# Performance work log

Hardware: AMD Instinct MI355X
Metric: run time of the kernel (lower is better)

## Reference

```python
import jax, jax.numpy as jnp
import numpy as np

N = 32768
F0, F1, F2, F3 = 16, 32, 64, 128
D0, D1, D2, D3 = (128, 128, 128), (64, 64, 64), (32, 32, 32), (16, 16, 16)
DST1, DST2, DTF = (16, 16, 16, 64), (64, 64, 32, 16), (4, 4, 4, 65536)
FST1, FST2, FTF = 64, 8, 8
TOTAL = 7 * (F0 + F1 + F2 + F3) + 9 * FST1 + 9 * FST2 + FTF  # 2336
INNER = 64
FACE3 = np.array([[1,0,0],[-1,0,0],[0,1,0],[0,-1,0],[0,0,1],[0,0,-1]], np.int32)
ST8 = np.concatenate([np.concatenate([FACE3, np.zeros((6,1), np.int32)], 1),
                      np.array([[0,0,0,1],[0,0,0,-1]], np.int32)], 0)

def rmsnorm(x, scale, eps=1e-8):
    rms = jnp.sqrt(jnp.mean(x * x, axis=-1, keepdims=True))
    return scale * x / (rms + eps)

def geglu(x):
    a, g = jnp.split(x, 2, axis=-1)
    return a * jax.nn.gelu(g)

def table_feats(table, p, offsets):
    # p in [0,1)^D -> scaled integer indices; gather base + modulo-wrapped neighbors
    dims = np.array(table.shape[:-1], np.int32)
    idx = (p * (dims - 1)).astype(jnp.int32)  # [N, D]
    base = table[tuple(idx[:, i] for i in range(idx.shape[-1]))]  # [N, F]
    if offsets is None:
        return base
    nbr = (idx[:, None, :] + offsets[None]) % dims  # [N, K, D]
    nf = table[tuple(nbr[..., i] for i in range(nbr.shape[-1]))]  # [N, K, F]
    return jnp.concatenate([base, nf.reshape(nf.shape[0], -1)], axis=-1)

def setup_inputs():
    key = jax.random.key(0)
    ks = jax.random.split(key, 20)
    tbl = lambda k, dims, f: jax.random.normal(k, dims + (f,), jnp.float32) * 0.1
    lin = lambda k, i, o: jax.random.normal(k, (i, o), jnp.float32) / np.sqrt(i).astype(np.float32)
    return dict(
        pos=jax.random.normal(ks[0], (N, 3), jnp.float32),
        dir=jax.random.normal(ks[1], (N, 3), jnp.float32),
        t=jax.random.uniform(ks[2], (N,), jnp.float32),
        table0=tbl(ks[3], D0, F0), table1=tbl(ks[4], D1, F1),
        table2=tbl(ks[5], D2, F2), table3=tbl(ks[6], D3, F3),
        st1=tbl(ks[7], DST1, FST1), st2=tbl(ks[8], DST2, FST2), tf=tbl(ks[9], DTF, FTF),
        sph_proj=lin(ks[10], 3, 8), tb1=jnp.zeros((1,), jnp.float32), tb2=jnp.zeros((1,), jnp.float32),
        gn1=jnp.ones((12,), jnp.float32), gw1=lin(ks[11], 12, 32),
        gn2=jnp.ones((16,), jnp.float32), gw2=lin(ks[12], 16, 32),
        gn3=jnp.ones((16,), jnp.float32), gw3=lin(ks[13], 16, 3),
        vn1=jnp.ones((TOTAL,), jnp.float32), vw1=lin(ks[14], TOTAL, 2 * TOTAL),
        vn2=jnp.ones((TOTAL,), jnp.float32), vw2=lin(ks[15], TOTAL, INNER),
        fw=lin(ks[16], INNER + 4, 4), fb=jnp.zeros((4,), jnp.float32))

def _forward(pos, dir, t, table0, table1, table2, table3, st1, st2, tf,
             sph_proj, tb1, tb2, gn1, gw1, gn2, gw2, gn3, gw3,
             vn1, vw1, vn2, vw2, fw, fb):
    # SphericalEmbedding
    rho = jnp.sqrt(jnp.sum(pos * pos, axis=-1, keepdims=True))
    phi = jnp.arctan2(pos[:, 1], pos[:, 0])
    theta = jnp.arccos(jnp.clip(pos[:, 2] / rho[:, 0], -1.0, 1.0))
    sph = jnp.stack([rho[:, 0], phi, theta], axis=-1) @ sph_proj  # [N, 8]
    # TimeEmbedding
    ct = jnp.cos(t[:, None] + tb1)
    st_ = jnp.sin(t[:, None] + tb2)
    temb = jnp.concatenate([ct, st_, jax.nn.silu(ct), jax.nn.silu(st_)], axis=-1)  # [N, 4]
    # geometric projection MLP -> normalized lookup coords
    h = jnp.concatenate([sph, temb], axis=-1)  # [N, 12]
    h = geglu(rmsnorm(h, gn1) @ gw1)  # [N, 16]
    h = geglu(rmsnorm(h, gn2) @ gw2)  # [N, 16]
    p = jax.nn.sigmoid(rmsnorm(h, gn3) @ gw3)  # [N, 3] in (0,1)
    pt = jnp.concatenate([p, t[:, None]], axis=-1)  # [N, 4]
    # multi-resolution gathers: base + 6 face neighbors per spatial table
    allf = jnp.concatenate([
        table_feats(table0, p, FACE3), table_feats(table1, p, FACE3),
        table_feats(table2, p, FACE3), table_feats(table3, p, FACE3),
        table_feats(st1, pt, ST8), table_feats(st2, pt, ST8),
        table_feats(tf, pt, None)], axis=-1)  # [N, TOTAL]
    # value MLP
    v = geglu(rmsnorm(allf, vn1) @ vw1)  # [N, TOTAL]
    down = rmsnorm(v, vn2) @ vw2  # [N, INNER]
    final_in = jnp.concatenate([down, p, t[:, None]], axis=-1)  # [N, INNER+4]
    return final_in @ fw + fb  # [N, 4]

def reference(pos, dir, t, table0, table1, table2, table3, st1, st2, tf,
              sph_proj, tb1, tb2, gn1, gw1, gn2, gw2, gn3, gw3,
              vn1, vw1, vn2, vw2, fw, fb):
    return _forward(pos, dir, t, table0, table1, table2, table3, st1, st2, tf,
                    sph_proj, tb1, tb2, gn1, gw1, gn2, gw2, gn3, gw3,
                    vn1, vw1, vn2, vw2, fw, fb)
```

## Files before the change

kernel.cpp:

```cpp
#include <hip/hip_runtime.h>
#include <hip/hip_bf16.h>
#include <stdint.h>

typedef __hip_bfloat16 bf16;
typedef __attribute__((ext_vector_type(8))) short v8s;
typedef __attribute__((ext_vector_type(4))) float v4f;

#define NPTS 32768
#define KTOT 2336
#define MPH  2368
#define NBX  37

#define AS1C(p) ((const __attribute__((address_space(1))) void*)(p))
#define AS3(p)  ((__attribute__((address_space(3))) void*)(p))

__device__ __forceinline__ float sigm(float x){ return 1.0f/(1.0f + expf(-x)); }
__device__ __forceinline__ float gelu_tanh(float x){
  float u = 0.7978845608028654f*(x + 0.044715f*x*x*x);
  return 0.5f*x*(1.0f + tanhf(u));
}
__device__ __forceinline__ float gelu_fast(float x){
  float u = 1.5957691216057308f*x*(1.0f + 0.044715f*x*x);
  return x / (1.0f + __expf(-u));
}

__global__ __launch_bounds__(256) void k_preamble(
    const float* __restrict__ pos, const float* __restrict__ t,
    const float* __restrict__ sph_proj, const float* __restrict__ tb1,
    const float* __restrict__ tb2,
    const float* __restrict__ gn1, const float* __restrict__ gw1,
    const float* __restrict__ gn2, const float* __restrict__ gw2,
    const float* __restrict__ gn3, const float* __restrict__ gw3,
    float4* __restrict__ Pbuf)
{
  int i = blockIdx.x*256 + threadIdx.x;
  if(i >= NPTS) return;
  float px = pos[3*i], py = pos[3*i+1], pz = pos[3*i+2];
  float rho = sqrtf(px*px + py*py + pz*pz);
  float phi = atan2f(py, px);
  float cz = fminf(1.0f, fmaxf(-1.0f, pz/rho));
  float theta = acosf(cz);
  float tv = t[i];
  float h[12];
  #pragma unroll
  for(int j=0;j<8;j++)
    h[j] = rho*sph_proj[j] + phi*sph_proj[8+j] + theta*sph_proj[16+j];
  float ct = cosf(tv + tb1[0]);
  float st = sinf(tv + tb2[0]);
  h[8]=ct; h[9]=st; h[10]=ct*sigm(ct); h[11]=st*sigm(st);

  float ss = 0.f;
  #pragma unroll
  for(int j=0;j<12;j++) ss += h[j]*h[j];
  float den = sqrtf(ss/12.0f) + 1e-8f;
  float hn[12];
  #pragma unroll
  for(int j=0;j<12;j++) hn[j] = gn1[j]*h[j]/den;

  float h2[16];
  #pragma unroll
  for(int j=0;j<16;j++){
    float a=0.f, g=0.f;
    #pragma unroll
    for(int k=0;k<12;k++){ a += hn[k]*gw1[k*32+j]; g += hn[k]*gw1[k*32+16+j]; }
    h2[j] = a*gelu_tanh(g);
  }
  ss = 0.f;
  #pragma unroll
  for(int j=0;j<16;j++) ss += h2[j]*h2[j];
  den = sqrtf(ss/16.0f) + 1e-8f;
  float hn2[16];
  #pragma unroll
  for(int j=0;j<16;j++) hn2[j] = gn2[j]*h2[j]/den;

  float h3[16];
  #pragma unroll
  for(int j=0;j<16;j++){
    float a=0.f, g=0.f;
    #pragma unroll
    for(int k=0;k<16;k++){ a += hn2[k]*gw2[k*32+j]; g += hn2[k]*gw2[k*32+16+j]; }
    h3[j] = a*gelu_tanh(g);
  }
  ss = 0.f;
  #pragma unroll
  for(int j=0;j<16;j++) ss += h3[j]*h3[j];
  den = sqrtf(ss/16.0f) + 1e-8f;
  float q[3];
  #pragma unroll
  for(int j=0;j<3;j++){
    float a=0.f;
    #pragma unroll
    for(int k=0;k<16;k++) a += (gn3[k]*h3[k]/den)*gw3[k*3+j];
    q[j] = sigm(a);
  }
  Pbuf[i] = make_float4(q[0], q[1], q[2], tv);
}

template<int F, int R>
__device__ __forceinline__ float rows_copyT(const float* __restrict__ T,
    const int (&offs)[R], bf16* __restrict__ dst, int lane){
  float ss = 0.f;
  if constexpr (F >= 64){
    #pragma unroll
    for(int r=0;r<R;r++){
      #pragma unroll
      for(int f0=0; f0<F; f0+=64){
        float v = T[(size_t)offs[r] + f0 + lane];
        dst[r*F + f0 + lane] = __float2bfloat16(v);
        ss += v*v;
      }
    }
  } else {
    constexpr int RPP = 64/F;
    int sub = lane / F;
    int f   = lane & (F-1);
    #pragma unroll
    for(int r0=0;r0<R;r0+=RPP){
      int r = r0 + sub;
      if(r < R){
        float v = T[(size_t)offs[r] + f];
        dst[r*F + f] = __float2bfloat16(v);
        ss += v*v;
      }
    }
  }
  return ss;
}

template<int F>
__device__ __forceinline__ float table3_gather(const float* __restrict__ T, int d,
    float p0, float p1, float p2, bf16* __restrict__ dst, int lane){
  int ix = (int)(p0*(float)(d-1));
  int iy = (int)(p1*(float)(d-1));
  int iz = (int)(p2*(float)(d-1));
  int xp = (ix+1>=d)?0:ix+1, xm = (ix==0)?d-1:ix-1;
  int yp = (iy+1>=d)?0:iy+1, ym = (iy==0)?d-1:iy-1;
  int zp = (iz+1>=d)?0:iz+1, zm = (iz==0)?d-1:iz-1;
  int offs[7] = {
    ((ix*d+iy)*d+iz)*F, ((xp*d+iy)*d+iz)*F, ((xm*d+iy)*d+iz)*F,
    ((ix*d+yp)*d+iz)*F, ((ix*d+ym)*d+iz)*F,
    ((ix*d+iy)*d+zp)*F, ((ix*d+iy)*d+zm)*F };
  return rows_copyT<F,7>(T, offs, dst, lane);
}

template<int F>
__device__ __forceinline__ float table4_gather(const float* __restrict__ T,
    int d0,int d1,int d2,int d3,
    float p0,float p1,float p2,float p3, bf16* __restrict__ dst, int lane){
  int ix = (int)(p0*(float)(d0-1));
  int iy = (int)(p1*(float)(d1-1));
  int iz = (int)(p2*(float)(d2-1));
  int iw = (int)(p3*(float)(d3-1));
  int xp=(ix+1>=d0)?0:ix+1, xm=(ix==0)?d0-1:ix-1;
  int yp=(iy+1>=d1)?0:iy+1, ym=(iy==0)?d1-1:iy-1;
  int zp=(iz+1>=d2)?0:iz+1, zm=(iz==0)?d2-1:iz-1;
  int wp=(iw+1>=d3)?0:iw+1, wm=(iw==0)?d3-1:iw-1;
  #define RO(x,y,z,w) (((((x)*d1 + (y))*d2 + (z))*d3 + (w))*F)
  int offs[9] = {
    RO(ix,iy,iz,iw), RO(xp,iy,iz,iw), RO(xm,iy,iz,iw),
    RO(ix,yp,iz,iw), RO(ix,ym,iz,iw), RO(ix,iy,zp,iw), RO(ix,iy,zm,iw),
    RO(ix,iy,iz,wp), RO(ix,iy,iz,wm) };
  #undef RO
  return rows_copyT<F,9>(T, offs, dst, lane);
}

__global__ __launch_bounds__(256) void k_gather(
    const float4* __restrict__ Pbuf,
    const float* __restrict__ T0, const float* __restrict__ T1,
    const float* __restrict__ T2, const float* __restrict__ T3,
    const float* __restrict__ S1, const float* __restrict__ S2,
    const float* __restrict__ TF,
    bf16* __restrict__ X, float* __restrict__ sx)
{
  int wave = threadIdx.x>>6, lane = threadIdx.x&63;
  int ptid = blockIdx.x*4 + wave;
  float4 P = Pbuf[ptid];
  bf16* dst = X + (size_t)ptid*KTOT;
  float ss = 0.f;
  ss += table3_gather<16 >(T0, 128, P.x, P.y, P.z, dst + 0,    lane);
  ss += table3_gather<32 >(T1,  64, P.x, P.y, P.z, dst + 112,  lane);
  ss += table3_gather<64 >(T2,  32, P.x, P.y, P.z, dst + 336,  lane);
  ss += table3_gather<128>(T3,  16, P.x, P.y, P.z, dst + 784,  lane);
  ss += table4_gather<64>(S1, 16,16,16,64, P.x,P.y,P.z,P.w, dst + 1680, lane);
  ss += table4_gather<8 >(S2, 64,64,32,16, P.x,P.y,P.z,P.w, dst + 2256, lane);
  {
    int ix=(int)(P.x*3.0f), iy=(int)(P.y*3.0f), iz=(int)(P.z*3.0f);
    int iw=(int)(P.w*65535.0f);
    int offs[1] = { (int)((((ix*4+iy)*4+iz))*65536 + iw)*8 };
    ss += rows_copyT<8,1>(TF, offs, dst + 2328, lane);
  }
  #pragma unroll
  for(int o=32;o>0;o>>=1) ss += __shfl_xor(ss, o);
  if(lane==0) sx[ptid] = 1.0f/(sqrtf(ss/2336.0f) + 1e-8f);
}

__global__ __launch_bounds__(256) void k_w1prep(const float* __restrict__ vw1,
                                                const float* __restrict__ vn1,
                                                bf16* __restrict__ W1b)
{
  __shared__ float tile[32][33];
  int h  = blockIdx.z;
  int m0 = blockIdx.x*32, k0 = blockIdx.y*32;
  int tx = threadIdx.x & 31, ty = threadIdx.x >> 5;
  #pragma unroll
  for(int dy=0; dy<32; dy+=8){
    int k = k0 + ty + dy;
    tile[ty+dy][tx] = vw1[(size_t)k*4672 + h*2336 + m0 + tx] * vn1[k];
  }
  __syncthreads();
  #pragma unroll
  for(int dy=0; dy<32; dy+=8){
    int m = m0 + ty + dy;
    W1b[(size_t)(h*MPH + m)*KTOT + k0 + tx] = __float2bfloat16(tile[tx][ty+dy]);
  }
}

__global__ __launch_bounds__(256) void k_w1pad(bf16* __restrict__ W1b){
  int idx = blockIdx.x*256 + threadIdx.x;
  const int total = 2*32*KTOT;
  if(idx >= total) return;
  int h = idx / (32*KTOT);
  int r = idx % (32*KTOT);
  int m = 2336 + r / KTOT;
  int k = r % KTOT;
  W1b[(size_t)(h*MPH + m)*KTOT + k] = __float2bfloat16(0.0f);
}

__global__ __launch_bounds__(256) void k_w2prep(const float* __restrict__ vw2,
                                                const float* __restrict__ vn2,
                                                const float* __restrict__ fw,
                                                float4* __restrict__ W2f)
{
  int k = blockIdx.x*256 + threadIdx.x;
  if(k >= KTOT) return;
  float a0=0,a1=0,a2=0,a3=0;
  for(int i=0;i<64;i++){
    float w = vw2[k*64+i];
    a0 += w*fw[i*4+0]; a1 += w*fw[i*4+1]; a2 += w*fw[i*4+2]; a3 += w*fw[i*4+3];
  }
  float s = vn2[k];
  W2f[k] = make_float4(s*a0, s*a1, s*a2, s*a3);
}

__global__ __launch_bounds__(256) void k_gemm1(
    const bf16* __restrict__ X, const bf16* __restrict__ W1b,
    const float* __restrict__ sx, const float4* __restrict__ W2f,
    float* __restrict__ Part)
{
  __shared__ bf16 As[128*32];
  __shared__ bf16 Bs[2*64*32];
  int tid = threadIdx.x;
  int wave = tid>>6, lane = tid&63;
  int bx = blockIdx.x, by = blockIdx.y;
  int row0 = by*128;
  int colh = bx*64;
  int wm = wave>>1, wn = wave&1;
  int lm = lane&15, lq = lane>>4;

  v4f acc[2][4][2];
  #pragma unroll
  for(int h=0;h<2;h++)
    #pragma unroll
    for(int i=0;i<4;i++)
      #pragma unroll
      for(int j=0;j<2;j++)
        acc[h][i][j] = (v4f){0.f,0.f,0.f,0.f};

  const bf16* Xb  = X   + (size_t)row0*KTOT;
  const bf16* Wb0 = W1b + (size_t)colh*KTOT;
  const bf16* Wb1 = W1b + (size_t)(MPH + colh)*KTOT;

  int arow0 = (0*256+tid)>>2, aq0 = ((0*256+tid)&3) ^ (((0*256+tid)>>3)&3);
  int arow1 = (1*256+tid)>>2, aq1 = ((1*256+tid)&3) ^ (((1*256+tid)>>3)&3);
  int brow  = tid>>2,         bq  = (tid&3) ^ ((tid>>3)&3);

  int aoff[4], boff[2];
  #pragma unroll
  for(int i=0;i<4;i++){
    int r = wm*64 + i*16 + lm;
    aoff[i] = (r*4 + (lq ^ ((r>>1)&3)))*8;
  }
  #pragma unroll
  for(int j=0;j<2;j++){
    int r = wn*32 + j*16 + lm;
    boff[j] = (r*4 + (lq ^ ((r>>1)&3)))*8;
  }

  for(int k0=0; k0<KTOT; k0+=32){
    {
      const bf16* g0 = Xb + (size_t)arow0*KTOT + k0 + aq0*8;
      __builtin_amdgcn_global_load_lds(AS1C(g0), AS3(As + (size_t)(wave*64)*8), 16, 0, 0);
      const bf16* g1 = Xb + (size_t)arow1*KTOT + k0 + aq1*8;
      __builtin_amdgcn_global_load_lds(AS1C(g1), AS3(As + (size_t)(256 + wave*64)*8), 16, 0, 0);
      const bf16* g2 = Wb0 + (size_t)brow*KTOT + k0 + bq*8;
      __builtin_amdgcn_global_load_lds(AS1C(g2), AS3(Bs + (size_t)(wave*64)*8), 16, 0, 0);
      const bf16* g3 = Wb1 + (size_t)brow*KTOT + k0 + bq*8;
      __builtin_amdgcn_global_load_lds(AS1C(g3), AS3(Bs + (size_t)(256 + wave*64)*8), 16, 0, 0);
    }
    __syncthreads();

    v8s af[4], ba[2], bg[2];
    #pragma unroll
    for(int i=0;i<4;i++) af[i] = *(const v8s*)(As + aoff[i]);
    #pragma unroll
    for(int j=0;j<2;j++){
      ba[j] = *(const v8s*)(Bs + boff[j]);
      bg[j] = *(const v8s*)(Bs + 2048 + boff[j]);
    }
    #pragma unroll
    for(int i=0;i<4;i++)
      #pragma unroll
      for(int j=0;j<2;j++){
        acc[0][i][j] = __builtin_amdgcn_mfma_f32_16x16x32_bf16(af[i], ba[j], acc[0][i][j], 0,0,0);
        acc[1][i][j] = __builtin_amdgcn_mfma_f32_16x16x32_bf16(af[i], bg[j], acc[1][i][j], 0,0,0);
      }
    __syncthreads();
  }

  float* red = (float*)As;
  #pragma unroll
  for(int ph=0; ph<2; ph++){
    if(wn == ph){
      #pragma unroll
      for(int i=0;i<4;i++){
        #pragma unroll
        for(int r=0;r<4;r++){
          int lrow = wm*64 + i*16 + lq*4 + r;
          float s = sx[row0 + lrow];
          float d0=0,d1=0,d2=0,d3=0,ssq=0;
          #pragma unroll
          for(int j=0;j<2;j++){
            int gcol = colh + wn*32 + j*16 + lm;
            float va = s*acc[0][i][j][r];
            float vg = s*acc[1][i][j][r];
            float v  = va * gelu_fast(vg);
            int ci = gcol < KTOT ? gcol : KTOT-1;
            float4 w = W2f[ci];
            d0 += v*w.x; d1 += v*w.y; d2 += v*w.z; d3 += v*w.w;
            ssq += v*v;
          }
          #pragma unroll
          for(int o=1;o<16;o<<=1){
            d0 += __shfl_xor(d0,o); d1 += __shfl_xor(d1,o);
            d2 += __shfl_xor(d2,o); d3 += __shfl_xor(d3,o);
            ssq += __shfl_xor(ssq,o);
          }
          if(lm==0){
            if(ph==0){
              red[lrow*8+0]=d0; red[lrow*8+1]=d1; red[lrow*8+2]=d2;
              red[lrow*8+3]=d3; red[lrow*8+4]=ssq;
              red[lrow*8+5]=0.f; red[lrow*8+6]=0.f; red[lrow*8+7]=0.f;
            } else {
              red[lrow*8+0]+=d0; red[lrow*8+1]+=d1; red[lrow*8+2]+=d2;
              red[lrow*8+3]+=d3; red[lrow*8+4]+=ssq;
            }
          }
        }
      }
    }
    __syncthreads();
  }
  {
    int rr = tid >> 1, c4 = (tid & 1)*4;
    float4 val = *(float4*)&red[rr*8 + c4];
    *(float4*)&Part[((size_t)bx*NPTS + row0 + rr)*8 + c4] = val;
  }
}

__global__ __launch_bounds__(256) void k_finalize(const float* __restrict__ Part,
    const float4* __restrict__ Pbuf, const float* __restrict__ fw,
    const float* __restrict__ fb, float4* __restrict__ out)
{
  int row = blockIdx.x*256 + threadIdx.x;
  const float4* P4 = (const float4*)Part;
  float d0=0,d1=0,d2=0,d3=0,ss=0;
  for(int bx=0; bx<NBX; bx++){
    size_t base = ((size_t)bx*NPTS + row)*2;
    float4 a = P4[base];
    float4 b = P4[base+1];
    d0+=a.x; d1+=a.y; d2+=a.z; d3+=a.w; ss+=b.x;
  }
  float sv = 1.0f/(sqrtf(ss/2336.0f)+1e-8f);
  float4 P = Pbuf[row];
  float o0 = sv*d0 + P.x*fw[256+0] + P.y*fw[260+0] + P.z*fw[264+0] + P.w*fw[268+0] + fb[0];
  float o1 = sv*d1 + P.x*fw[256+1] + P.y*fw[260+1] + P.z*fw[264+1] + P.w*fw[268+1] + fb[1];
  float o2 = sv*d2 + P.x*fw[256+2] + P.y*fw[260+2] + P.z*fw[264+2] + P.w*fw[268+2] + fb[2];
  float o3 = sv*d3 + P.x*fw[256+3] + P.y*fw[260+3] + P.z*fw[264+3] + P.w*fw[268+3] + fb[3];
  out[row] = make_float4(o0,o1,o2,o3);
}

extern "C" void kernel_launch(void* const* d_in, const int* in_sizes, int n_in,
                              void* d_out, int out_size, void* d_ws, size_t ws_size,
                              hipStream_t stream)
{
  const float* pos = (const float*)d_in[0];
  const float* t   = (const float*)d_in[2];
  const float* T0  = (const float*)d_in[3];
  const float* T1  = (const float*)d_in[4];
  const float* T2  = (const float*)d_in[5];
  const float* T3  = (const float*)d_in[6];
  const float* S1  = (const float*)d_in[7];
  const float* S2  = (const float*)d_in[8];
  const float* TF  = (const float*)d_in[9];
  const float* sph = (const float*)d_in[10];
  const float* tb1 = (const float*)d_in[11];
  const float* tb2 = (const float*)d_in[12];
  const float* gn1 = (const float*)d_in[13];
  const float* gw1 = (const float*)d_in[14];
  const float* gn2 = (const float*)d_in[15];
  const float* gw2 = (const float*)d_in[16];
  const float* gn3 = (const float*)d_in[17];
  const float* gw3 = (const float*)d_in[18];
  const float* vn1 = (const float*)d_in[19];
  const float* vw1 = (const float*)d_in[20];
  const float* vn2 = (const float*)d_in[21];
  const float* vw2 = (const float*)d_in[22];
  const float* fw  = (const float*)d_in[23];
  const float* fb  = (const float*)d_in[24];

  uint8_t* ws = (uint8_t*)d_ws;
  size_t off = 0;
  auto carve = [&](size_t bytes)->void*{
    void* pp = ws + off; off += (bytes + 255) & ~(size_t)255; return pp;
  };
  float4* Pbuf = (float4*)carve((size_t)NPTS*sizeof(float4));
  float*  sx   = (float*) carve((size_t)NPTS*sizeof(float));
  float4* W2f  = (float4*)carve((size_t)KTOT*sizeof(float4));
  bf16*   W1b  = (bf16*)  carve((size_t)2*MPH*KTOT*sizeof(bf16));
  bf16*   X    = (bf16*)  carve((size_t)NPTS*KTOT*sizeof(bf16));
  float*  Part = (float*) carve((size_t)NBX*NPTS*8*sizeof(float));

  k_preamble<<<NPTS/256, 256, 0, stream>>>(pos, t, sph, tb1, tb2,
                                           gn1, gw1, gn2, gw2, gn3, gw3, Pbuf);
  k_gather<<<NPTS/4, 256, 0, stream>>>(Pbuf, T0, T1, T2, T3, S1, S2, TF, X, sx);
  k_w1prep<<<dim3(73,73,2), 256, 0, stream>>>(vw1, vn1, W1b);
  k_w1pad<<<(2*32*KTOT + 255)/256, 256, 0, stream>>>(W1b);
  k_w2prep<<<(KTOT + 255)/256, 256, 0, stream>>>(vw2, vn2, fw, W2f);
  k_gemm1<<<dim3(NBX, 256), 256, 0, stream>>>(X, W1b, sx, W2f, Part);
  k_finalize<<<NPTS/256, 256, 0, stream>>>(Part, Pbuf, fw, fb, (float4*)d_out);
}
```

Before: 1.795 ms.

## Enlarge GEMM tile to 256x128 with 4-stage async LDS pipeline

The main GEMM moves from 128x64 tiles with 256 threads and a single synchronous LDS buffer to 256x128 tiles with 512 threads. It adds a 4-deep ring of LDS buffers filled by global_load_lds, uses explicit vmcnt waits so loads overlap MFMA work, and swizzles block IDs to improve L2 locality. Padding to 2432 columns is now done with a full zeroing kernel in place of the pad kernel, and the number of column blocks (partial sums) drops from 37 to 19. The risks are higher LDS use (128KB per block) and register pressure, which could limit occupancy, plus extra wasted work on the padded columns.

```diff
diff --git a/kernel.cpp b/kernel.cpp
--- a/kernel.cpp
+++ b/kernel.cpp
@@ -8,8 +8,8 @@
 
 #define NPTS 32768
 #define KTOT 2336
-#define MPH  2368
-#define NBX  37
+#define MPH2 2432
+#define NBX2 19
 
 #define AS1C(p) ((const __attribute__((address_space(1))) void*)(p))
 #define AS3(p)  ((__attribute__((address_space(3))) void*)(p))
@@ -194,6 +194,13 @@
   if(lane==0) sx[ptid] = 1.0f/(sqrtf(ss/2336.0f) + 1e-8f);
 }
 
+#define W1B_U4 ((2*MPH2*KTOT*2)/16)
+__global__ __launch_bounds__(256) void k_w1zero(uint4* __restrict__ W1b){
+  size_t idx = (size_t)blockIdx.x*256 + threadIdx.x;
+  if(idx < (size_t)W1B_U4)
+    W1b[idx] = make_uint4(0u,0u,0u,0u);
+}
+
 __global__ __launch_bounds__(256) void k_w1prep(const float* __restrict__ vw1,
                                                 const float* __restrict__ vn1,
                                                 bf16* __restrict__ W1b)
@@ -211,19 +218,8 @@
   #pragma unroll
   for(int dy=0; dy<32; dy+=8){
     int m = m0 + ty + dy;
-    W1b[(size_t)(h*MPH + m)*KTOT + k0 + tx] = __float2bfloat16(tile[tx][ty+dy]);
-  }
-}
-
-__global__ __launch_bounds__(256) void k_w1pad(bf16* __restrict__ W1b){
-  int idx = blockIdx.x*256 + threadIdx.x;
-  const int total = 2*32*KTOT;
-  if(idx >= total) return;
-  int h = idx / (32*KTOT);
-  int r = idx % (32*KTOT);
-  int m = 2336 + r / KTOT;
-  int k = r % KTOT;
-  W1b[(size_t)(h*MPH + m)*KTOT + k] = __float2bfloat16(0.0f);
+    W1b[(size_t)(h*MPH2 + m)*KTOT + k0 + tx] = __float2bfloat16(tile[tx][ty+dy]);
+  }
 }
 
 __global__ __launch_bounds__(256) void k_w2prep(const float* __restrict__ vw2,
@@ -242,99 +238,114 @@
   W2f[k] = make_float4(s*a0, s*a1, s*a2, s*a3);
 }
 
-__global__ __launch_bounds__(256) void k_gemm1(
+
+#define PIPE_WAIT(NSTR) do{                                   \
+    __builtin_amdgcn_sched_barrier(0);                        \
+    asm volatile("s_waitcnt vmcnt(" NSTR ")" ::: "memory");   \
+    __builtin_amdgcn_s_barrier();                             \
+  }while(0)
+
+template<int SB>
+__device__ __forceinline__ void stage4(const bf16* aSrc, const bf16* bSrc, int k0e,
+    bf16 (&As)[4][8192], bf16 (&Bs)[4][8192], int wave)
+{
+  __builtin_amdgcn_global_load_lds(AS1C(aSrc + k0e),            AS3(&As[SB][wave*512]),        16, 0, 0);
+  __builtin_amdgcn_global_load_lds(AS1C(aSrc + 128*KTOT + k0e), AS3(&As[SB][4096 + wave*512]), 16, 0, 0);
+  __builtin_amdgcn_global_load_lds(AS1C(bSrc + k0e),            AS3(&Bs[SB][wave*512]),        16, 0, 0);
+  __builtin_amdgcn_global_load_lds(AS1C(bSrc + 64*KTOT + k0e),  AS3(&Bs[SB][4096 + wave*512]), 16, 0, 0);
+}
+
+template<int RB, int SB, bool STG>
+__device__ __forceinline__ void body(const bf16* aSrc, const bf16* bSrc, int k0e,
+    bf16 (&As)[4][8192], bf16 (&Bs)[4][8192], int wave, int aOff, int bOff,
+    v4f (&acc)[8][4])
+{
+  v8s af[8]; v8s bb[4];
+  #pragma unroll
+  for(int i=0;i<8;i++) af[i] = *(const v8s*)(&As[RB][aOff + i*512]);
+  #pragma unroll
+  for(int j=0;j<4;j++) bb[j] = *(const v8s*)(&Bs[RB][bOff + j*512]);
+  if constexpr (STG) stage4<SB>(aSrc, bSrc, k0e, As, Bs, wave);
+  #pragma unroll
+  for(int i=0;i<8;i++)
+    #pragma unroll
+    for(int j=0;j<4;j++)
+      acc[i][j] = __builtin_amdgcn_mfma_f32_16x16x32_bf16(af[i], bb[j], acc[i][j], 0,0,0);
+}
+
+__global__ __launch_bounds__(512, 2) void k_gemm1(
     const bf16* __restrict__ X, const bf16* __restrict__ W1b,
     const float* __restrict__ sx, const float4* __restrict__ W2f,
     float* __restrict__ Part)
 {
-  __shared__ bf16 As[128*32];
-  __shared__ bf16 Bs[2*64*32];
+  __shared__ bf16 As[4][8192];
+  __shared__ bf16 Bs[4][8192];
   int tid = threadIdx.x;
   int wave = tid>>6, lane = tid&63;
-  int bx = blockIdx.x, by = blockIdx.y;
-  int row0 = by*128;
-  int colh = bx*64;
-  int wm = wave>>1, wn = wave&1;
+
+  int lid = blockIdx.x + 19*blockIdx.y;
+  int swz = (lid & 7)*304 + (lid >> 3);
+  int bx = swz % 19;
+  int by = swz / 19;
+  int row0 = by*256;
+  int colh = bx*128;
+
+  int wm = wave>>2, wn = wave&3;
   int lm = lane&15, lq = lane>>4;
 
-  v4f acc[2][4][2];
-  #pragma unroll
-  for(int h=0;h<2;h++)
-    #pragma unroll
-    for(int i=0;i<4;i++)
-      #pragma unroll
-      for(int j=0;j<2;j++)
-        acc[h][i][j] = (v4f){0.f,0.f,0.f,0.f};
-
-  const bf16* Xb  = X   + (size_t)row0*KTOT;
-  const bf16* Wb0 = W1b + (size_t)colh*KTOT;
-  const bf16* Wb1 = W1b + (size_t)(MPH + colh)*KTOT;
-
-  int arow0 = (0*256+tid)>>2, aq0 = ((0*256+tid)&3) ^ (((0*256+tid)>>3)&3);
-  int arow1 = (1*256+tid)>>2, aq1 = ((1*256+tid)&3) ^ (((1*256+tid)>>3)&3);
-  int brow  = tid>>2,         bq  = (tid&3) ^ ((tid>>3)&3);
-
-  int aoff[4], boff[2];
-  #pragma unroll
-  for(int i=0;i<4;i++){
-    int r = wm*64 + i*16 + lm;
-    aoff[i] = (r*4 + (lq ^ ((r>>1)&3)))*8;
-  }
-  #pragma unroll
-  for(int j=0;j<2;j++){
-    int r = wn*32 + j*16 + lm;
-    boff[j] = (r*4 + (lq ^ ((r>>1)&3)))*8;
-  }
-
-  for(int k0=0; k0<KTOT; k0+=32){
-    {
-      const bf16* g0 = Xb + (size_t)arow0*KTOT + k0 + aq0*8;
-      __builtin_amdgcn_global_load_lds(AS1C(g0), AS3(As + (size_t)(wave*64)*8), 16, 0, 0);
-      const bf16* g1 = Xb + (size_t)arow1*KTOT + k0 + aq1*8;
-      __builtin_amdgcn_global_load_lds(AS1C(g1), AS3(As + (size_t)(256 + wave*64)*8), 16, 0, 0);
-      const bf16* g2 = Wb0 + (size_t)brow*KTOT + k0 + bq*8;
-      __builtin_amdgcn_global_load_lds(AS1C(g2), AS3(Bs + (size_t)(wave*64)*8), 16, 0, 0);
-      const bf16* g3 = Wb1 + (size_t)brow*KTOT + k0 + bq*8;
-      __builtin_amdgcn_global_load_lds(AS1C(g3), AS3(Bs + (size_t)(256 + wave*64)*8), 16, 0, 0);
-    }
-    __syncthreads();
-
-    v8s af[4], ba[2], bg[2];
-    #pragma unroll
-    for(int i=0;i<4;i++) af[i] = *(const v8s*)(As + aoff[i]);
-    #pragma unroll
-    for(int j=0;j<2;j++){
-      ba[j] = *(const v8s*)(Bs + boff[j]);
-      bg[j] = *(const v8s*)(Bs + 2048 + boff[j]);
-    }
-    #pragma unroll
-    for(int i=0;i<4;i++)
-      #pragma unroll
-      for(int j=0;j<2;j++){
-        acc[0][i][j] = __builtin_amdgcn_mfma_f32_16x16x32_bf16(af[i], ba[j], acc[0][i][j], 0,0,0);
-        acc[1][i][j] = __builtin_amdgcn_mfma_f32_16x16x32_bf16(af[i], bg[j], acc[1][i][j], 0,0,0);
-      }
-    __syncthreads();
-  }
-
-  float* red = (float*)As;
-  #pragma unroll
-  for(int ph=0; ph<2; ph++){
+  v4f acc[8][4];
+  #pragma unroll
+  for(int i=0;i<8;i++)
+    #pragma unroll
+    for(int j=0;j<4;j++)
+      acc[i][j] = (v4f){0.f,0.f,0.f,0.f};
+
+  int r0 = tid>>2;
+  int qa = (tid&3) ^ ((tid>>3)&3);
+  const bf16* aSrc = X + (size_t)(row0 + r0)*KTOT + qa*8;
+  const bf16* bSrc = W1b + (size_t)(((r0>>5)&1)*MPH2 + colh + (r0>>6)*32 + (r0&31))*KTOT + qa*8;
+
+  int swz4 = lq ^ ((lm>>1)&3);
+  int aOff = ((wm*128 + lm)*4 + swz4)*8;
+  int bOff = ((wn*64  + lm)*4 + swz4)*8;
+
+  stage4<0>(aSrc, bSrc, 0,  As, Bs, wave);
+  stage4<1>(aSrc, bSrc, 32, As, Bs, wave);
+  stage4<2>(aSrc, bSrc, 64, As, Bs, wave);
+  PIPE_WAIT("8");
+
+  for(int t=0; t<68; t+=4){
+    int ke = (t+3)*32;
+    body<0,3,true>(aSrc,bSrc,ke,    As,Bs,wave,aOff,bOff,acc); PIPE_WAIT("8");
+    body<1,0,true>(aSrc,bSrc,ke+32, As,Bs,wave,aOff,bOff,acc); PIPE_WAIT("8");
+    body<2,1,true>(aSrc,bSrc,ke+64, As,Bs,wave,aOff,bOff,acc); PIPE_WAIT("8");
+    body<3,2,true>(aSrc,bSrc,ke+96, As,Bs,wave,aOff,bOff,acc); PIPE_WAIT("8");
+  }
+  body<0,3,true >(aSrc,bSrc,71*32, As,Bs,wave,aOff,bOff,acc); PIPE_WAIT("8");
+  body<1,0,true >(aSrc,bSrc,72*32, As,Bs,wave,aOff,bOff,acc); PIPE_WAIT("8");
+  body<2,0,false>(aSrc,bSrc,0,     As,Bs,wave,aOff,bOff,acc); PIPE_WAIT("4");
+  body<3,0,false>(aSrc,bSrc,0,     As,Bs,wave,aOff,bOff,acc); PIPE_WAIT("0");
+  body<0,0,false>(aSrc,bSrc,0,     As,Bs,wave,aOff,bOff,acc);
+  __syncthreads();
+
+  float* red = (float*)&As[0][0];
+  #pragma unroll
+  for(int ph=0; ph<4; ph++){
     if(wn == ph){
       #pragma unroll
-      for(int i=0;i<4;i++){
+      for(int i=0;i<8;i++){
         #pragma unroll
         for(int r=0;r<4;r++){
-          int lrow = wm*64 + i*16 + lq*4 + r;
+          int lrow = wm*128 + i*16 + lq*4 + r;
           float s = sx[row0 + lrow];
           float d0=0,d1=0,d2=0,d3=0,ssq=0;
           #pragma unroll
           for(int j=0;j<2;j++){
-            int gcol = colh + wn*32 + j*16 + lm;
-            float va = s*acc[0][i][j][r];
-            float vg = s*acc[1][i][j][r];
+            int c = colh + wn*32 + j*16 + lm;
+            float va = s*acc[i][j][r];
+            float vg = s*acc[i][j+2][r];
             float v  = va * gelu_fast(vg);
-            int ci = gcol < KTOT ? gcol : KTOT-1;
+            int ci = c < KTOT ? c : KTOT-1;
             float4 w = W2f[ci];
             d0 += v*w.x; d1 += v*w.y; d2 += v*w.z; d3 += v*w.w;
             ssq += v*v;
@@ -374,7 +385,7 @@
   int row = blockIdx.x*256 + threadIdx.x;
   const float4* P4 = (const float4*)Part;
   float d0=0,d1=0,d2=0,d3=0,ss=0;
-  for(int bx=0; bx<NBX; bx++){
+  for(int bx=0; bx<NBX2; bx++){
     size_t base = ((size_t)bx*NPTS + row)*2;
     float4 a = P4[base];
     float4 b = P4[base+1];
@@ -426,16 +437,16 @@
   float4* Pbuf = (float4*)carve((size_t)NPTS*sizeof(float4));
   float*  sx   = (float*) carve((size_t)NPTS*sizeof(float));
   float4* W2f  = (float4*)carve((size_t)KTOT*sizeof(float4));
-  bf16*   W1b  = (bf16*)  carve((size_t)2*MPH*KTOT*sizeof(bf16));
+  bf16*   W1b  = (bf16*)  carve((size_t)2*MPH2*KTOT*sizeof(bf16));
   bf16*   X    = (bf16*)  carve((size_t)NPTS*KTOT*sizeof(bf16));
-  float*  Part = (float*) carve((size_t)NBX*NPTS*8*sizeof(float));
+  float*  Part = (float*) carve((size_t)NBX2*NPTS*8*sizeof(float));
 
   k_preamble<<<NPTS/256, 256, 0, stream>>>(pos, t, sph, tb1, tb2,
                                            gn1, gw1, gn2, gw2, gn3, gw3, Pbuf);
+  k_w1zero<<<(W1B_U4 + 255)/256, 256, 0, stream>>>((uint4*)W1b);
+  k_w1prep<<<dim3(73,73,2), 256, 0, stream>>>(vw1, vn1, W1b);
+  k_w2prep<<<(KTOT + 255)/256, 256, 0, stream>>>(vw2, vn2, fw, W2f);
   k_gather<<<NPTS/4, 256, 0, stream>>>(Pbuf, T0, T1, T2, T3, S1, S2, TF, X, sx);
-  k_w1prep<<<dim3(73,73,2), 256, 0, stream>>>(vw1, vn1, W1b);
-  k_w1pad<<<(2*32*KTOT + 255)/256, 256, 0, stream>>>(W1b);
-  k_w2prep<<<(KTOT + 255)/256, 256, 0, stream>>>(vw2, vn2, fw, W2f);
-  k_gemm1<<<dim3(NBX, 256), 256, 0, stream>>>(X, W1b, sx, W2f, Part);
+  k_gemm1<<<dim3(19,128), 512, 0, stream>>>(X, W1b, sx, W2f, Part);
   k_finalize<<<NPTS/256, 256, 0, stream>>>(Part, Pbuf, fw, fb, (float4*)d_out);
 }
```

After: 1.614 ms. 1.11x faster.
